# Kernel tuning notes

Measured on AMD Instinct MI355X. Metric: run time of the kernel, lower is better.

Reference implementation:

```python
import jax, jax.numpy as jnp
import numpy as np

B, N_IN, N_MFS, N_RULES = 8192, 8, 4, 2048


def setup_inputs() -> dict:
    key = jax.random.key(0)
    k1, k2 = jax.random.split(key)
    # fuzzified membership values in [0, 1): (n_cases, n_in, n_mfs)
    x = jax.random.uniform(k1, (B, N_IN, N_MFS), dtype=jnp.float32)
    # rule MF-index table: values in [-1, n_mfs-1]; -1 means 'variable unused in rule'
    mf_indices = jax.random.randint(k2, (N_RULES, N_IN), 0, N_MFS + 1, dtype=jnp.int32) - 1
    return {"x": x, "mf_indices": mf_indices}


def reference(x, mf_indices):
    """AntecedentLayer.forward, rules path with AND_p (product t-norm).
    x:          (B, n_in, n_mfs)
    mf_indices: (n_rules, n_in), -1 = masked
    returns fire strengths: (B, n_rules)
    """
    cond = mf_indices == -1                      # (R, n_in)
    safe_idx = jnp.where(cond, 0, mf_indices)    # clamp sentinel for gather
    n_in = x.shape[1]
    # ants[b, r, i] = x[b, i, safe_idx[r, i]]  -> (B, R, n_in)
    ants = x[:, jnp.arange(n_in)[None, :], safe_idx]
    # masked variables contribute identity (1.0) to the product t-norm
    ants = jnp.where(cond[None, :, :], jnp.float32(1.0), ants)
    return jnp.prod(ants, axis=2)                # (B, R)
```

## Files before the change

kernel.cpp:

```cpp
#include <hip/hip_runtime.h>

#define B        8192
#define N_IN     8
#define N_MFS    4
#define N_RULES  2048

#define THREADS  256
#define NB       32
#define RSPLIT   8
#define RPB      (N_RULES / RSPLIT)
#define LUT_W    101
#define XS_W     (N_IN * N_MFS)

__global__ __launch_bounds__(THREADS) void fire_kernel(
        const float* __restrict__ x,
        const int*   __restrict__ mf,
        float* __restrict__ out)
{
    __shared__ float xs[NB * XS_W];
    __shared__ float slut[NB * LUT_W];

    const int tid = threadIdx.x;
    const int rg  = blockIdx.x;
    const int bg  = blockIdx.y;
    const int b0  = bg * NB;
    const int r   = rg * RPB + tid;

    {
        const float4* xg = (const float4*)(x + (size_t)b0 * XS_W);
        ((float4*)xs)[tid] = xg[tid];
    }

    int woff[4];
    {
        const int4* mr = (const int4*)(mf + (size_t)r * N_IN);
        const int4 lo = mr[0];
        const int4 hi = mr[1];
        const int idx[8] = {lo.x, lo.y, lo.z, lo.w, hi.x, hi.y, hi.z, hi.w};
#pragma unroll
        for (int p = 0; p < 4; ++p) {
            const int a = idx[2*p]   < 0 ? 4 : idx[2*p];
            const int b = idx[2*p+1] < 0 ? 4 : idx[2*p+1];
            woff[p] = p * 25 + a * 5 + b;
        }
    }
    __syncthreads();

    for (int e = tid; e < NB * 100; e += THREADS) {
        const int bl   = e / 100;
        const int rest = e - bl * 100;
        const int p    = rest / 25;
        const int c    = rest - p * 25;
        const int a    = c / 5;
        const int bb   = c - a * 5;
        const float* xb = xs + bl * XS_W;
        const float va = (a  < 4) ? xb[(2*p)   * N_MFS + a ] : 1.0f;
        const float vb = (bb < 4) ? xb[(2*p+1) * N_MFS + bb] : 1.0f;
        slut[bl * LUT_W + rest] = va * vb;
    }
    __syncthreads();

    float* o = out + (size_t)b0 * N_RULES + r;
#pragma unroll 8
    for (int bl = 0; bl < NB; ++bl) {
        const float* lb = slut + bl * LUT_W;
        const float v0 = lb[woff[0]];
        const float v1 = lb[woff[1]];
        const float v2 = lb[woff[2]];
        const float v3 = lb[woff[3]];
        o[(size_t)bl * N_RULES] = (v0 * v1) * (v2 * v3);
    }
}

extern "C" void kernel_launch(void* const* d_in, const int* in_sizes, int n_in,
                              void* d_out, int out_size, void* d_ws, size_t ws_size,
                              hipStream_t stream) {
    const float* x  = (const float*)d_in[0];
    const int*   mf = (const int*)d_in[1];
    float* out = (float*)d_out;
    (void)d_ws; (void)ws_size;

    dim3 grid(RSPLIT, B / NB);
    fire_kernel<<<grid, THREADS, 0, stream>>>(x, mf, out);
}
```

Before: 83.75 us.

## Give each thread four consecutive rules with vectorized float4 output stores

Restructures the work split so each block covers all rules for 16 batch rows, with each thread handling four adjacent rules and writing them as a float4. This cuts the number of scalar global stores and the redundant per-block LUT construction across rule splits. In exchange, each block re-reads the full rule table, keeps more offsets in registers, and the grid shrinks to fewer blocks, which may lower occupancy and latency hiding.

```diff
diff --git a/kernel.cpp b/kernel.cpp
--- a/kernel.cpp
+++ b/kernel.cpp
@@ -5,10 +5,9 @@
 #define N_MFS    4
 #define N_RULES  2048
 
-#define THREADS  256
-#define NB       32
-#define RSPLIT   8
-#define RPB      (N_RULES / RSPLIT)
+#define THREADS  512
+#define NB       16
+#define RPT      4
 #define LUT_W    101
 #define XS_W     (N_IN * N_MFS)
 
@@ -21,18 +20,16 @@
     __shared__ float slut[NB * LUT_W];
 
     const int tid = threadIdx.x;
-    const int rg  = blockIdx.x;
-    const int bg  = blockIdx.y;
-    const int b0  = bg * NB;
-    const int r   = rg * RPB + tid;
+    const int b0  = blockIdx.x * NB;
 
-    {
-        const float4* xg = (const float4*)(x + (size_t)b0 * XS_W);
-        ((float4*)xs)[tid] = xg[tid];
+    if (tid < (NB * XS_W) / 4) {
+        ((float4*)xs)[tid] = ((const float4*)(x + (size_t)b0 * XS_W))[tid];
     }
 
-    int woff[4];
-    {
+    int woff[RPT][4];
+#pragma unroll
+    for (int j = 0; j < RPT; ++j) {
+        const int r = tid * RPT + j;
         const int4* mr = (const int4*)(mf + (size_t)r * N_IN);
         const int4 lo = mr[0];
         const int4 hi = mr[1];
@@ -41,7 +38,7 @@
         for (int p = 0; p < 4; ++p) {
             const int a = idx[2*p]   < 0 ? 4 : idx[2*p];
             const int b = idx[2*p+1] < 0 ? 4 : idx[2*p+1];
-            woff[p] = p * 25 + a * 5 + b;
+            woff[j][p] = p * 25 + a * 5 + b;
         }
     }
     __syncthreads();
@@ -60,15 +57,32 @@
     }
     __syncthreads();
 
-    float* o = out + (size_t)b0 * N_RULES + r;
-#pragma unroll 8
+#pragma unroll 2
     for (int bl = 0; bl < NB; ++bl) {
         const float* lb = slut + bl * LUT_W;
-        const float v0 = lb[woff[0]];
-        const float v1 = lb[woff[1]];
-        const float v2 = lb[woff[2]];
-        const float v3 = lb[woff[3]];
-        o[(size_t)bl * N_RULES] = (v0 * v1) * (v2 * v3);
+        float r0, r1, r2, r3;
+        {
+            const float v0 = lb[woff[0][0]], v1 = lb[woff[0][1]];
+            const float v2 = lb[woff[0][2]], v3 = lb[woff[0][3]];
+            r0 = (v0 * v1) * (v2 * v3);
+        }
+        {
+            const float v0 = lb[woff[1][0]], v1 = lb[woff[1][1]];
+            const float v2 = lb[woff[1][2]], v3 = lb[woff[1][3]];
+            r1 = (v0 * v1) * (v2 * v3);
+        }
+        {
+            const float v0 = lb[woff[2][0]], v1 = lb[woff[2][1]];
+            const float v2 = lb[woff[2][2]], v3 = lb[woff[2][3]];
+            r2 = (v0 * v1) * (v2 * v3);
+        }
+        {
+            const float v0 = lb[woff[3][0]], v1 = lb[woff[3][1]];
+            const float v2 = lb[woff[3][2]], v3 = lb[woff[3][3]];
+            r3 = (v0 * v1) * (v2 * v3);
+        }
+        *(float4*)(out + (size_t)(b0 + bl) * N_RULES + tid * RPT) =
+            make_float4(r0, r1, r2, r3);
     }
 }
 
@@ -80,6 +94,5 @@
     float* out = (float*)d_out;
     (void)d_ws; (void)ws_size;
 
-    dim3 grid(RSPLIT, B / NB);
-    fire_kernel<<<grid, THREADS, 0, stream>>>(x, mf, out);
+    fire_kernel<<<B / NB, THREADS, 0, stream>>>(x, mf, out);
 }
```

After: 94.45 us. 1.13x slower.

## Compute two rules per thread with vectorized nontemporal stores and smaller batch tile

Applied to the files above, without the earlier changes.

Each thread now computes two adjacent rules and writes them as one float2 nontemporal store, with the batch tile reduced from 32 to 16 and rule splits from 8 to 4. The per-block LUT build covers fewer batch rows, so its cost is spread over more rules per block, and the output writes become wider and bypass cache. Using more registers for two offset sets, and having more blocks each rebuild the LUT for fewer rows, may shift occupancy and redundant work.

```diff
diff --git a/kernel.cpp b/kernel.cpp
--- a/kernel.cpp
+++ b/kernel.cpp
@@ -6,11 +6,13 @@
 #define N_RULES  2048
 
 #define THREADS  256
-#define NB       32
-#define RSPLIT   8
+#define NB       16
+#define RSPLIT   4
 #define RPB      (N_RULES / RSPLIT)
 #define LUT_W    101
 #define XS_W     (N_IN * N_MFS)
+
+typedef float vfloat2 __attribute__((ext_vector_type(2)));
 
 __global__ __launch_bounds__(THREADS) void fire_kernel(
         const float* __restrict__ x,
@@ -24,16 +26,16 @@
     const int rg  = blockIdx.x;
     const int bg  = blockIdx.y;
     const int b0  = bg * NB;
-    const int r   = rg * RPB + tid;
+    const int r0  = rg * RPB + tid * 2;
 
-    {
-        const float4* xg = (const float4*)(x + (size_t)b0 * XS_W);
-        ((float4*)xs)[tid] = xg[tid];
+    if (tid < (NB * XS_W) / 4) {
+        ((float4*)xs)[tid] = ((const float4*)(x + (size_t)b0 * XS_W))[tid];
     }
 
-    int woff[4];
-    {
-        const int4* mr = (const int4*)(mf + (size_t)r * N_IN);
+    int woff[2][4];
+#pragma unroll
+    for (int j = 0; j < 2; ++j) {
+        const int4* mr = (const int4*)(mf + (size_t)(r0 + j) * N_IN);
         const int4 lo = mr[0];
         const int4 hi = mr[1];
         const int idx[8] = {lo.x, lo.y, lo.z, lo.w, hi.x, hi.y, hi.z, hi.w};
@@ -41,7 +43,7 @@
         for (int p = 0; p < 4; ++p) {
             const int a = idx[2*p]   < 0 ? 4 : idx[2*p];
             const int b = idx[2*p+1] < 0 ? 4 : idx[2*p+1];
-            woff[p] = p * 25 + a * 5 + b;
+            woff[j][p] = p * 25 + a * 5 + b;
         }
     }
     __syncthreads();
@@ -60,15 +62,22 @@
     }
     __syncthreads();
 
-    float* o = out + (size_t)b0 * N_RULES + r;
-#pragma unroll 8
+    float* o = out + (size_t)b0 * N_RULES + rg * RPB + tid * 2;
+#pragma unroll 4
     for (int bl = 0; bl < NB; ++bl) {
         const float* lb = slut + bl * LUT_W;
-        const float v0 = lb[woff[0]];
-        const float v1 = lb[woff[1]];
-        const float v2 = lb[woff[2]];
-        const float v3 = lb[woff[3]];
-        o[(size_t)bl * N_RULES] = (v0 * v1) * (v2 * v3);
+        vfloat2 res;
+        {
+            const float v0 = lb[woff[0][0]], v1 = lb[woff[0][1]];
+            const float v2 = lb[woff[0][2]], v3 = lb[woff[0][3]];
+            res.x = (v0 * v1) * (v2 * v3);
+        }
+        {
+            const float v0 = lb[woff[1][0]], v1 = lb[woff[1][1]];
+            const float v2 = lb[woff[1][2]], v3 = lb[woff[1][3]];
+            res.y = (v0 * v1) * (v2 * v3);
+        }
+        __builtin_nontemporal_store(res, (vfloat2*)(o + (size_t)bl * N_RULES));
     }
 }
 
```

After: 79.85 us. 1.05x faster.
